# Performance work log

Hardware: AMD Instinct MI355X
Metric: run time of the kernel (lower is better)

Reference implementation:

```python
import jax, jax.numpy as jnp
import numpy as np

N_NODES = 10000
N_RAND_EDGES = 320000
IN_DIM = 256
HIDDEN = 64
HEADS = 8
OUT_DIM = 256
NEG_SLOPE = 0.2


def setup_inputs() -> dict:
    key = jax.random.key(0)
    ks = jax.random.split(key, 9)
    h = jax.random.normal(ks[0], (N_NODES, IN_DIM), dtype=jnp.float32)
    # random edges + self-loops so every dst has >=1 incoming edge
    src = jnp.concatenate([
        jax.random.randint(ks[1], (N_RAND_EDGES,), 0, N_NODES, dtype=jnp.int32),
        jnp.arange(N_NODES, dtype=jnp.int32)])
    dst = jnp.concatenate([
        jax.random.randint(ks[2], (N_RAND_EDGES,), 0, N_NODES, dtype=jnp.int32),
        jnp.arange(N_NODES, dtype=jnp.int32)])
    def glorot(k, shape):
        fan = shape[0] + shape[-1]
        s = jnp.sqrt(2.0 / fan).astype(jnp.float32)
        return jax.random.normal(k, shape, dtype=jnp.float32) * s
    W1 = glorot(ks[3], (IN_DIM, HEADS * HIDDEN))
    attn_l1 = glorot(ks[4], (HEADS, HIDDEN))
    attn_r1 = glorot(ks[5], (HEADS, HIDDEN))
    W2 = glorot(ks[6], (HEADS * HIDDEN, OUT_DIM))
    attn_l2 = glorot(ks[7], (1, OUT_DIM))
    attn_r2 = glorot(ks[8], (1, OUT_DIM))
    return {"h": h, "W1": W1, "attn_l1": attn_l1, "attn_r1": attn_r1,
            "W2": W2, "attn_l2": attn_l2, "attn_r2": attn_r2,
            "src": src, "dst": dst}


def gat_conv(x, W, attn_l, attn_r, src, dst, n_nodes):
    # x: [N, F_in]; W: [F_in, H*D]; attn_l/attn_r: [H, D]
    H, D = attn_l.shape
    feat = (x @ W).reshape(n_nodes, H, D)          # [N, H, D]
    el = jnp.einsum('nhd,hd->nh', feat, attn_l)    # [N, H]
    er = jnp.einsum('nhd,hd->nh', feat, attn_r)
    e = jax.nn.leaky_relu(el[src] + er[dst], NEG_SLOPE)  # [E, H]
    # edge softmax over incoming edges of each destination node
    m = jax.ops.segment_max(e, dst, num_segments=n_nodes)      # [N, H]
    ex = jnp.exp(e - m[dst])                                   # [E, H]
    denom = jax.ops.segment_sum(ex, dst, num_segments=n_nodes) # [N, H]
    alpha = ex / denom[dst]                                    # [E, H]
    out = jax.ops.segment_sum(alpha[:, :, None] * feat[src], dst,
                              num_segments=n_nodes)            # [N, H, D]
    return out.reshape(n_nodes, H * D)


def reference(h, W1, attn_l1, attn_r1, W2, attn_l2, attn_r2, src, dst):
    n = h.shape[0]
    x = gat_conv(h, W1, attn_l1, attn_r1, src, dst, n)   # [N, H*hidden]
    x = jax.nn.elu(x)
    out = gat_conv(x, W2, attn_l2, attn_r2, src, dst, n) # [N, out_dim]
    return out
```

## Files before the change

kernel.cpp:

```cpp
#include <hip/hip_runtime.h>
#include <hip/hip_bf16.h>

#define N_NODES 10000
#define IN_DIM 256
#define HID 512
#define HEADS 8
#define OUT_DIM 256
#define NEG 0.2f
#define CAP 128
#define WPREP_BLOCKS (((IN_DIM*HID)+(HID*OUT_DIM))/256)

typedef __hip_bfloat16 bf16;
typedef __attribute__((ext_vector_type(8))) short short8;
typedef __attribute__((ext_vector_type(4))) float f32x4;

__device__ __forceinline__ float ldm(const void* p, long i, int mode){
  if(mode) return ((const float*)p)[i];
  return __bfloat162float(((const bf16*)p)[i]);
}
__device__ __forceinline__ unsigned short f2bf(float f){
  bf16 b = __float2bfloat16(f);
  return *(unsigned short*)&b;
}
__device__ __forceinline__ float bflo(unsigned int u){ return __uint_as_float(u<<16); }
__device__ __forceinline__ float bfhi(unsigned int u){ return __uint_as_float(u&0xffff0000u); }

__global__ void detect_zero_k(const unsigned short* w1raw, int* mode, int* cnt,
                              float* el2, float* er2){
  int t = threadIdx.x;
  if(blockIdx.x==0){
    __shared__ int sbad;
    if(t==0) sbad=0;
    __syncthreads();
    int bad=0;
    for(int i=t;i<512;i+=256){
      unsigned int u = ((unsigned int)w1raw[i])<<16;
      float f = __uint_as_float(u);
      if(!(f==f) || fabsf(f) > 100.0f) bad++;
    }
    #pragma unroll
    for(int o=32;o>0;o>>=1) bad += __shfl_down(bad,o);
    if((t&63)==0) atomicAdd(&sbad, bad);
    __syncthreads();
    if(t==0) *mode = (sbad>10) ? 1 : 0;
  } else {
    int i = (blockIdx.x-1)*256 + t;
    if(i<N_NODES){ cnt[i]=0; el2[i]=0.f; er2[i]=0.f; }
  }
}

__global__ void prep2_k(const void* W1, const void* W2, unsigned short* wt1,
                        unsigned short* wt2, const int* modep,
                        const int* src, const int* dst, int* cnt, int* bucket, int E){
  int b = blockIdx.x, t = threadIdx.x;
  if(b < WPREP_BLOCKS){
    int md = *modep;
    long i = (long)b*256 + t;
    const long n1 = (long)IN_DIM*HID;
    if(i < n1){
      int k = (int)(i/HID), n = (int)(i%HID);
      unsigned short v = md ? f2bf(((const float*)W1)[i]) : ((const unsigned short*)W1)[i];
      wt1[(long)n*IN_DIM + k] = v;
    } else {
      long j = i - n1;
      int k = (int)(j/OUT_DIM), n = (int)(j%OUT_DIM);
      unsigned short v = md ? f2bf(((const float*)W2)[j]) : ((const unsigned short*)W2)[j];
      wt2[(long)n*HID + k] = v;
    }
  } else {
    int e = (b-WPREP_BLOCKS)*256 + t;
    if(e<E){
      int d = dst[e];
      int pos = atomicAdd(&cnt[d], 1);
      if(pos < CAP) bucket[(long)d*CAP + pos] = src[e];
    }
  }
}

__global__ __launch_bounds__(256) void gemm_k(const void* A, const unsigned short* Bt,
                                              unsigned short* C, int M, int N, int K,
                                              int asel, const int* modep,
                                              const void* al, const void* ar,
                                              float* el, float* er, int dmode){
  int md = *modep;
  int am = asel ? md : 0;
  __shared__ short As[64*40];
  __shared__ short Bs[64*40];
  __shared__ float led[64], ler[64];
  int t = threadIdx.x;
  int lane = t & 63, wave = t >> 6;
  int l15 = lane & 15, quad = lane >> 4;
  int wm = (wave>>1)*32, wn = (wave&1)*32;
  int mbase = blockIdx.y*64, nbase = blockIdx.x*64;

  f32x4 acc[2][2];
  #pragma unroll
  for(int i=0;i<2;i++)
    #pragma unroll
    for(int j=0;j<2;j++) acc[i][j] = (f32x4){0.f,0.f,0.f,0.f};

  int row = t>>2, kk = (t&3)*8;
  long arow = (long)(mbase+row)*K, brow = (long)(nbase+row)*K;
  bool av = (mbase+row) < M;
  const unsigned short* Ab = (const unsigned short*)A;
  const float* Af = (const float*)A;

  for(int k0=0;k0<K;k0+=32){
    short8 a = (short8){0,0,0,0,0,0,0,0};
    if(am){
      if(av){
        float4 x = *(const float4*)(Af + arow + k0 + kk);
        float4 y = *(const float4*)(Af + arow + k0 + kk + 4);
        a[0]=f2bf(x.x); a[1]=f2bf(x.y); a[2]=f2bf(x.z); a[3]=f2bf(x.w);
        a[4]=f2bf(y.x); a[5]=f2bf(y.y); a[6]=f2bf(y.z); a[7]=f2bf(y.w);
      }
    } else {
      if(av) a = *(const short8*)(Ab + arow + k0 + kk);
    }
    short8 b = *(const short8*)(Bt + brow + k0 + kk);
    __syncthreads();
    *(short8*)(As + row*40 + kk) = a;
    *(short8*)(Bs + row*40 + kk) = b;
    __syncthreads();
    short8 af[2], bfr[2];
    #pragma unroll
    for(int mi=0;mi<2;mi++) af[mi]  = *(short8*)(As + (wm + mi*16 + l15)*40 + quad*8);
    #pragma unroll
    for(int ni=0;ni<2;ni++) bfr[ni] = *(short8*)(Bs + (wn + ni*16 + l15)*40 + quad*8);
    #pragma unroll
    for(int mi=0;mi<2;mi++)
      #pragma unroll
      for(int ni=0;ni<2;ni++)
        acc[mi][ni] = __builtin_amdgcn_mfma_f32_16x16x32_bf16(af[mi], bfr[ni], acc[mi][ni], 0,0,0);
  }

  #pragma unroll
  for(int mi=0;mi<2;mi++){
    #pragma unroll
    for(int ni=0;ni<2;ni++){
      int grow0 = mbase + wm + mi*16 + quad*4;
      int gcol  = nbase + wn + ni*16 + l15;
      #pragma unroll
      for(int r=0;r<4;r++){
        int grow = grow0 + r;
        if(grow < M) C[(long)grow*N + gcol] = f2bf(acc[mi][ni][r]);
      }
    }
  }

  float avv[2], rvv[2];
  #pragma unroll
  for(int ni=0;ni<2;ni++){
    int gc = nbase + wn + ni*16 + l15;
    avv[ni] = ldm(al, gc, md);
    rvv[ni] = ldm(ar, gc, md);
  }
  __syncthreads();
  if(t<64){ led[t]=0.f; ler[t]=0.f; }
  __syncthreads();
  #pragma unroll
  for(int mi=0;mi<2;mi++){
    #pragma unroll
    for(int r=0;r<4;r++){
      float pl = acc[mi][0][r]*avv[0] + acc[mi][1][r]*avv[1];
      float pr = acc[mi][0][r]*rvv[0] + acc[mi][1][r]*rvv[1];
      #pragma unroll
      for(int o=1;o<16;o<<=1){ pl += __shfl_xor(pl,o); pr += __shfl_xor(pr,o); }
      if(l15==0){
        int lr = wm + mi*16 + quad*4 + r;
        atomicAdd(&led[lr], pl);
        atomicAdd(&ler[lr], pr);
      }
    }
  }
  __syncthreads();
  if(t<64){
    int grow = mbase + t;
    if(grow < M){
      if(dmode==1){
        el[(long)grow*HEADS + blockIdx.x] = led[t];
        er[(long)grow*HEADS + blockIdx.x] = ler[t];
      } else {
        atomicAdd(&el[grow], led[t]);
        atomicAdd(&er[grow], ler[t]);
      }
    }
  }
}

__global__ __launch_bounds__(64) void agg1_k(const unsigned short* fb, const float* el,
                       const float* er, const int* cnt, const int* bucket, unsigned short* x){
  int b = blockIdx.x;
  int ch = b / N_NODES;
  int n  = b - ch*N_NODES;
  int t = threadIdx.x;
  long off = (long)n*CAP;
  int deg = cnt[n]; if(deg>CAP) deg=CAP;
  __shared__ int sidx[CAP];
  __shared__ float wl[4][CAP];
  for(int i=t;i<deg;i+=64) sidx[i]=bucket[off+i];
  __syncthreads();
  int h0 = ch*4;
  float4 erv = *(const float4*)(er + (long)n*HEADS + h0);
  float pw0=0.f, pw1=0.f, pw2=0.f, pw3=0.f;
  for(int i=t;i<deg;i+=64){
    int s = sidx[i];
    float4 ev = *(const float4*)(el + (long)s*HEADS + h0);
    float e0 = ev.x + erv.x; e0 = e0>0.f?e0:NEG*e0;
    float e1 = ev.y + erv.y; e1 = e1>0.f?e1:NEG*e1;
    float e2 = ev.z + erv.z; e2 = e2>0.f?e2:NEG*e2;
    float e3 = ev.w + erv.w; e3 = e3>0.f?e3:NEG*e3;
    float wa = __expf(e0), wb = __expf(e1), wc = __expf(e2), wd = __expf(e3);
    wl[0][i]=wa; wl[1][i]=wb; wl[2][i]=wc; wl[3][i]=wd;
    pw0+=wa; pw1+=wb; pw2+=wc; pw3+=wd;
  }
  #pragma unroll
  for(int o=32;o>0;o>>=1){
    pw0 += __shfl_xor(pw0,o); pw1 += __shfl_xor(pw1,o);
    pw2 += __shfl_xor(pw2,o); pw3 += __shfl_xor(pw3,o);
  }
  float invs[4];
  invs[0] = pw0>0.f?1.f/pw0:0.f; invs[1] = pw1>0.f?1.f/pw1:0.f;
  invs[2] = pw2>0.f?1.f/pw2:0.f; invs[3] = pw3>0.f?1.f/pw3:0.f;
  __syncthreads();
  int hl = t>>4;
  int c0 = ch*256 + 4*t;
  const float* wsel = wl[hl];
  float inv = invs[hl];
  float a0=0.f,a1=0.f,a2=0.f,a3=0.f;
  #pragma unroll 4
  for(int i=0;i<deg;i++){
    int s = sidx[i];
    float w = wsel[i];
    uint2 u = *(const uint2*)(fb + (long)s*HID + c0);
    a0 += w*bflo(u.x); a1 += w*bfhi(u.x);
    a2 += w*bflo(u.y); a3 += w*bfhi(u.y);
  }
  a0*=inv; a1*=inv; a2*=inv; a3*=inv;
  a0 = a0>0.f ? a0 : __expf(a0)-1.f;
  a1 = a1>0.f ? a1 : __expf(a1)-1.f;
  a2 = a2>0.f ? a2 : __expf(a2)-1.f;
  a3 = a3>0.f ? a3 : __expf(a3)-1.f;
  uint2 o2;
  o2.x = (unsigned int)f2bf(a0) | ((unsigned int)f2bf(a1)<<16);
  o2.y = (unsigned int)f2bf(a2) | ((unsigned int)f2bf(a3)<<16);
  *(uint2*)(x + (long)n*HID + c0) = o2;
}

__global__ __launch_bounds__(64) void agg2_k(const unsigned short* fb, const float* el,
                       const float* er, const int* cnt, const int* bucket, void* out,
                       const int* modep){
  int md = *modep;
  int n = blockIdx.x, t = threadIdx.x;
  long off = (long)n*CAP;
  int deg = cnt[n]; if(deg>CAP) deg=CAP;
  __shared__ int sidx[CAP];
  __shared__ float wl[CAP];
  for(int i=t;i<deg;i+=64) sidx[i]=bucket[off+i];
  __syncthreads();
  float ern = er[n];
  float pw = 0.f;
  for(int i=t;i<deg;i+=64){
    int s = sidx[i];
    float e = el[s]+ern; e = e>0.f ? e : NEG*e;
    float w = __expf(e);
    wl[i]=w;
    pw += w;
  }
  #pragma unroll
  for(int o=32;o>0;o>>=1) pw += __shfl_xor(pw,o);
  float inv = pw>0.f ? 1.f/pw : 0.f;
  __syncthreads();
  int c0 = 4*t;
  float a0=0.f,a1=0.f,a2=0.f,a3=0.f;
  #pragma unroll 4
  for(int i=0;i<deg;i++){
    int s = sidx[i];
    float w = wl[i];
    uint2 u = *(const uint2*)(fb + (long)s*OUT_DIM + c0);
    a0 += w*bflo(u.x); a1 += w*bfhi(u.x);
    a2 += w*bflo(u.y); a3 += w*bfhi(u.y);
  }
  a0*=inv; a1*=inv; a2*=inv; a3*=inv;
  long oi = (long)n*OUT_DIM + c0;
  if(md){
    float4 fo; fo.x=a0; fo.y=a1; fo.z=a2; fo.w=a3;
    *(float4*)((float*)out + oi) = fo;
  } else {
    uint2 o2;
    o2.x = (unsigned int)f2bf(a0) | ((unsigned int)f2bf(a1)<<16);
    o2.y = (unsigned int)f2bf(a2) | ((unsigned int)f2bf(a3)<<16);
    *(uint2*)((unsigned short*)out + oi) = o2;
  }
}

extern "C" void kernel_launch(void* const* d_in, const int* in_sizes, int n_in,
                              void* d_out, int out_size, void* d_ws, size_t ws_size,
                              hipStream_t stream){
  (void)n_in; (void)out_size; (void)ws_size;
  const void* h_in = d_in[0];
  const void* W1   = d_in[1];
  const void* al1  = d_in[2];
  const void* ar1  = d_in[3];
  const void* W2   = d_in[4];
  const void* al2  = d_in[5];
  const void* ar2  = d_in[6];
  const int* src = (const int*)d_in[7];
  const int* dst = (const int*)d_in[8];
  int E = in_sizes[7];

  char* ws = (char*)d_ws;
  size_t o = 0;
  auto alloc = [&](size_t b){ size_t c=o; o += (b+255)&~(size_t)255; return c; };
  unsigned short* f1b  = (unsigned short*)(ws + alloc((size_t)N_NODES*HID*2));
  unsigned short* f2b  = (unsigned short*)(ws + alloc((size_t)N_NODES*OUT_DIM*2));
  unsigned short* xbuf = (unsigned short*)(ws + alloc((size_t)N_NODES*HID*2));
  unsigned short* wt1  = (unsigned short*)(ws + alloc((size_t)IN_DIM*HID*2));
  unsigned short* wt2  = (unsigned short*)(ws + alloc((size_t)HID*OUT_DIM*2));
  float* el1   = (float*)(ws + alloc((size_t)N_NODES*HEADS*4));
  float* er1   = (float*)(ws + alloc((size_t)N_NODES*HEADS*4));
  float* el2   = (float*)(ws + alloc((size_t)N_NODES*4));
  float* er2   = (float*)(ws + alloc((size_t)N_NODES*4));
  int* cnt     = (int*)(ws + alloc((size_t)N_NODES*4));
  int* bucket  = (int*)(ws + alloc((size_t)N_NODES*CAP*4));
  int* modep   = (int*)(ws + alloc(256));

  detect_zero_k<<<1+(N_NODES+255)/256,256,0,stream>>>(
      (const unsigned short*)W1, modep, cnt, el2, er2);
  prep2_k<<<WPREP_BLOCKS+(E+255)/256,256,0,stream>>>(
      W1, W2, wt1, wt2, modep, src, dst, cnt, bucket, E);

  gemm_k<<<dim3(HID/64,(N_NODES+63)/64),256,0,stream>>>(
      h_in, wt1, f1b, N_NODES, HID, IN_DIM, 1, modep, al1, ar1, el1, er1, 1);
  agg1_k<<<2*N_NODES,64,0,stream>>>(f1b, el1, er1, cnt, bucket, xbuf);

  gemm_k<<<dim3(OUT_DIM/64,(N_NODES+63)/64),256,0,stream>>>(
      xbuf, wt2, f2b, N_NODES, OUT_DIM, HID, 0, modep, al2, ar2, el2, er2, 2);
  agg2_k<<<N_NODES,64,0,stream>>>(f2b, el2, er2, cnt, bucket, d_out, modep);
}
```

Before: 184.1 us.

## Tile weight transpose through LDS and widen aggregation gathers to 16-byte loads

The weight-prep transpose now moves 64x64 tiles through shared memory with vectorized loads and stores, replacing the old uncoalesced scalar scatter. agg1 now runs one 128-thread block per node covering all 8 heads, where it used to run two 64-thread blocks per node. Each lane gathers 8 bf16 values with uint4 loads, the two waves split the edge list, and their partials are combined through LDS. agg2 also splits its edges across two half-waves with 16-byte loads and a shuffle reduction. This aims for fewer, wider gather transactions and less redundant edge-weight work, at the cost of fewer blocks and an extra reduction step.

```diff
diff --git a/kernel.cpp b/kernel.cpp
--- a/kernel.cpp
+++ b/kernel.cpp
@@ -8,7 +8,7 @@
 #define OUT_DIM 256
 #define NEG 0.2f
 #define CAP 128
-#define WPREP_BLOCKS (((IN_DIM*HID)+(HID*OUT_DIM))/256)
+#define WT_BLOCKS 64
 
 typedef __hip_bfloat16 bf16;
 typedef __attribute__((ext_vector_type(8))) short short8;
@@ -53,22 +53,43 @@
                         unsigned short* wt2, const int* modep,
                         const int* src, const int* dst, int* cnt, int* bucket, int E){
   int b = blockIdx.x, t = threadIdx.x;
-  if(b < WPREP_BLOCKS){
+  if(b < WT_BLOCKS){
     int md = *modep;
-    long i = (long)b*256 + t;
-    const long n1 = (long)IN_DIM*HID;
-    if(i < n1){
-      int k = (int)(i/HID), n = (int)(i%HID);
-      unsigned short v = md ? f2bf(((const float*)W1)[i]) : ((const unsigned short*)W1)[i];
-      wt1[(long)n*IN_DIM + k] = v;
+    __shared__ __align__(16) unsigned short tl[64*72];
+    int isW2 = (b>=32);
+    int bb = isW2 ? b-32 : b;
+    const void* W = isW2 ? W2 : W1;
+    unsigned short* wt = isW2 ? wt2 : wt1;
+    int K = isW2 ? HID : IN_DIM;
+    int N = isW2 ? OUT_DIM : HID;
+    int sh = isW2 ? 2 : 3;
+    int kt = bb >> sh, nt = bb & ((1<<sh)-1);
+    int r = t>>2, c0 = (t&3)<<4;
+    long srow = (long)(kt*64 + r)*N + nt*64 + c0;
+    unsigned short v[16] __attribute__((aligned(16)));
+    if(md){
+      const float* Wf = (const float*)W;
+      #pragma unroll
+      for(int j=0;j<16;j+=4){
+        float4 xv = *(const float4*)(Wf + srow + j);
+        v[j]=f2bf(xv.x); v[j+1]=f2bf(xv.y); v[j+2]=f2bf(xv.z); v[j+3]=f2bf(xv.w);
+      }
     } else {
-      long j = i - n1;
-      int k = (int)(j/OUT_DIM), n = (int)(j%OUT_DIM);
-      unsigned short v = md ? f2bf(((const float*)W2)[j]) : ((const unsigned short*)W2)[j];
-      wt2[(long)n*HID + k] = v;
-    }
+      const unsigned short* Wb = (const unsigned short*)W;
+      *(short8*)&v[0] = *(const short8*)(Wb+srow);
+      *(short8*)&v[8] = *(const short8*)(Wb+srow+8);
+    }
+    #pragma unroll
+    for(int j=0;j<16;j++) tl[(c0+j)*72 + r] = v[j];
+    __syncthreads();
+    int nn = t>>2, k0 = (t&3)<<4;
+    short8 o0 = *(short8*)&tl[nn*72+k0];
+    short8 o1 = *(short8*)&tl[nn*72+k0+8];
+    long drow = (long)(nt*64+nn)*K + kt*64 + k0;
+    *(short8*)(wt+drow)   = o0;
+    *(short8*)(wt+drow+8) = o1;
   } else {
-    int e = (b-WPREP_BLOCKS)*256 + t;
+    int e = (b-WT_BLOCKS)*256 + t;
     if(e<E){
       int d = dst[e];
       int pos = atomicAdd(&cnt[d], 1);
@@ -188,63 +209,92 @@
   }
 }
 
-__global__ __launch_bounds__(64) void agg1_k(const unsigned short* fb, const float* el,
+__global__ __launch_bounds__(128) void agg1_k(const unsigned short* fb, const float* el,
                        const float* er, const int* cnt, const int* bucket, unsigned short* x){
-  int b = blockIdx.x;
-  int ch = b / N_NODES;
-  int n  = b - ch*N_NODES;
+  int n = blockIdx.x;
   int t = threadIdx.x;
   long off = (long)n*CAP;
   int deg = cnt[n]; if(deg>CAP) deg=CAP;
   __shared__ int sidx[CAP];
-  __shared__ float wl[4][CAP];
-  for(int i=t;i<deg;i+=64) sidx[i]=bucket[off+i];
-  __syncthreads();
-  int h0 = ch*4;
-  float4 erv = *(const float4*)(er + (long)n*HEADS + h0);
-  float pw0=0.f, pw1=0.f, pw2=0.f, pw3=0.f;
-  for(int i=t;i<deg;i+=64){
+  __shared__ __align__(16) float swl[CAP*8];
+  __shared__ float pws[2][8];
+  __shared__ float sinv[8];
+  __shared__ __align__(16) float pacc[64][8];
+  for(int i=t;i<deg;i+=128) sidx[i]=bucket[off+i];
+  __syncthreads();
+  const float* erp = er + (long)n*HEADS;
+  float4 era = *(const float4*)erp, erb = *(const float4*)(erp+4);
+  float err8[8] = {era.x,era.y,era.z,era.w,erb.x,erb.y,erb.z,erb.w};
+  float pw[8];
+  #pragma unroll
+  for(int j=0;j<8;j++) pw[j]=0.f;
+  for(int i=t;i<deg;i+=128){
     int s = sidx[i];
-    float4 ev = *(const float4*)(el + (long)s*HEADS + h0);
-    float e0 = ev.x + erv.x; e0 = e0>0.f?e0:NEG*e0;
-    float e1 = ev.y + erv.y; e1 = e1>0.f?e1:NEG*e1;
-    float e2 = ev.z + erv.z; e2 = e2>0.f?e2:NEG*e2;
-    float e3 = ev.w + erv.w; e3 = e3>0.f?e3:NEG*e3;
-    float wa = __expf(e0), wb = __expf(e1), wc = __expf(e2), wd = __expf(e3);
-    wl[0][i]=wa; wl[1][i]=wb; wl[2][i]=wc; wl[3][i]=wd;
-    pw0+=wa; pw1+=wb; pw2+=wc; pw3+=wd;
-  }
-  #pragma unroll
-  for(int o=32;o>0;o>>=1){
-    pw0 += __shfl_xor(pw0,o); pw1 += __shfl_xor(pw1,o);
-    pw2 += __shfl_xor(pw2,o); pw3 += __shfl_xor(pw3,o);
-  }
-  float invs[4];
-  invs[0] = pw0>0.f?1.f/pw0:0.f; invs[1] = pw1>0.f?1.f/pw1:0.f;
-  invs[2] = pw2>0.f?1.f/pw2:0.f; invs[3] = pw3>0.f?1.f/pw3:0.f;
-  __syncthreads();
-  int hl = t>>4;
-  int c0 = ch*256 + 4*t;
-  const float* wsel = wl[hl];
-  float inv = invs[hl];
-  float a0=0.f,a1=0.f,a2=0.f,a3=0.f;
+    const float* ep = el + (long)s*HEADS;
+    float4 ea = *(const float4*)ep, eb = *(const float4*)(ep+4);
+    float ev[8] = {ea.x,ea.y,ea.z,ea.w,eb.x,eb.y,eb.z,eb.w};
+    float wv[8];
+    #pragma unroll
+    for(int j=0;j<8;j++){
+      float e = ev[j] + err8[j];
+      e = e>0.f ? e : NEG*e;
+      float w = __expf(e);
+      wv[j]=w; pw[j]+=w;
+    }
+    *(float4*)&swl[i*8]   = make_float4(wv[0],wv[1],wv[2],wv[3]);
+    *(float4*)&swl[i*8+4] = make_float4(wv[4],wv[5],wv[6],wv[7]);
+  }
+  #pragma unroll
+  for(int o=32;o>0;o>>=1)
+    #pragma unroll
+    for(int j=0;j<8;j++) pw[j]+=__shfl_xor(pw[j],o);
+  int wv_ = t>>6, l = t&63;
+  if(l==0){
+    #pragma unroll
+    for(int j=0;j<8;j++) pws[wv_][j]=pw[j];
+  }
+  __syncthreads();
+  if(t<8){ float s2 = pws[0][t]+pws[1][t]; sinv[t] = s2>0.f ? 1.f/s2 : 0.f; }
+  __syncthreads();
+  int h = l>>3;
+  int c0 = 8*l;
+  float a0=0.f,a1=0.f,a2=0.f,a3=0.f,a4=0.f,a5=0.f,a6=0.f,a7=0.f;
   #pragma unroll 4
-  for(int i=0;i<deg;i++){
+  for(int i=wv_; i<deg; i+=2){
     int s = sidx[i];
-    float w = wsel[i];
-    uint2 u = *(const uint2*)(fb + (long)s*HID + c0);
+    float w = swl[i*8+h];
+    uint4 u = *(const uint4*)(fb + (long)s*HID + c0);
     a0 += w*bflo(u.x); a1 += w*bfhi(u.x);
     a2 += w*bflo(u.y); a3 += w*bfhi(u.y);
-  }
-  a0*=inv; a1*=inv; a2*=inv; a3*=inv;
-  a0 = a0>0.f ? a0 : __expf(a0)-1.f;
-  a1 = a1>0.f ? a1 : __expf(a1)-1.f;
-  a2 = a2>0.f ? a2 : __expf(a2)-1.f;
-  a3 = a3>0.f ? a3 : __expf(a3)-1.f;
-  uint2 o2;
-  o2.x = (unsigned int)f2bf(a0) | ((unsigned int)f2bf(a1)<<16);
-  o2.y = (unsigned int)f2bf(a2) | ((unsigned int)f2bf(a3)<<16);
-  *(uint2*)(x + (long)n*HID + c0) = o2;
+    a4 += w*bflo(u.z); a5 += w*bfhi(u.z);
+    a6 += w*bflo(u.w); a7 += w*bfhi(u.w);
+  }
+  if(wv_==1){
+    *(float4*)&pacc[l][0] = make_float4(a0,a1,a2,a3);
+    *(float4*)&pacc[l][4] = make_float4(a4,a5,a6,a7);
+  }
+  __syncthreads();
+  if(wv_==0){
+    float4 q0 = *(float4*)&pacc[l][0], q1 = *(float4*)&pacc[l][4];
+    a0+=q0.x; a1+=q0.y; a2+=q0.z; a3+=q0.w;
+    a4+=q1.x; a5+=q1.y; a6+=q1.z; a7+=q1.w;
+    float inv = sinv[h];
+    a0*=inv; a1*=inv; a2*=inv; a3*=inv; a4*=inv; a5*=inv; a6*=inv; a7*=inv;
+    a0 = a0>0.f ? a0 : __expf(a0)-1.f;
+    a1 = a1>0.f ? a1 : __expf(a1)-1.f;
+    a2 = a2>0.f ? a2 : __expf(a2)-1.f;
+    a3 = a3>0.f ? a3 : __expf(a3)-1.f;
+    a4 = a4>0.f ? a4 : __expf(a4)-1.f;
+    a5 = a5>0.f ? a5 : __expf(a5)-1.f;
+    a6 = a6>0.f ? a6 : __expf(a6)-1.f;
+    a7 = a7>0.f ? a7 : __expf(a7)-1.f;
+    uint4 o4;
+    o4.x = (unsigned int)f2bf(a0) | ((unsigned int)f2bf(a1)<<16);
+    o4.y = (unsigned int)f2bf(a2) | ((unsigned int)f2bf(a3)<<16);
+    o4.z = (unsigned int)f2bf(a4) | ((unsigned int)f2bf(a5)<<16);
+    o4.w = (unsigned int)f2bf(a6) | ((unsigned int)f2bf(a7)<<16);
+    *(uint4*)(x + (long)n*HID + c0) = o4;
+  }
 }
 
 __global__ __launch_bounds__(64) void agg2_k(const unsigned short* fb, const float* el,
@@ -271,26 +321,39 @@
   for(int o=32;o>0;o>>=1) pw += __shfl_xor(pw,o);
   float inv = pw>0.f ? 1.f/pw : 0.f;
   __syncthreads();
-  int c0 = 4*t;
-  float a0=0.f,a1=0.f,a2=0.f,a3=0.f;
+  int half = t>>5, l = t&31;
+  int c0 = 8*l;
+  float a0=0.f,a1=0.f,a2=0.f,a3=0.f,a4=0.f,a5=0.f,a6=0.f,a7=0.f;
   #pragma unroll 4
-  for(int i=0;i<deg;i++){
+  for(int i=half; i<deg; i+=2){
     int s = sidx[i];
     float w = wl[i];
-    uint2 u = *(const uint2*)(fb + (long)s*OUT_DIM + c0);
+    uint4 u = *(const uint4*)(fb + (long)s*OUT_DIM + c0);
     a0 += w*bflo(u.x); a1 += w*bfhi(u.x);
     a2 += w*bflo(u.y); a3 += w*bfhi(u.y);
-  }
-  a0*=inv; a1*=inv; a2*=inv; a3*=inv;
-  long oi = (long)n*OUT_DIM + c0;
-  if(md){
-    float4 fo; fo.x=a0; fo.y=a1; fo.z=a2; fo.w=a3;
-    *(float4*)((float*)out + oi) = fo;
-  } else {
-    uint2 o2;
-    o2.x = (unsigned int)f2bf(a0) | ((unsigned int)f2bf(a1)<<16);
-    o2.y = (unsigned int)f2bf(a2) | ((unsigned int)f2bf(a3)<<16);
-    *(uint2*)((unsigned short*)out + oi) = o2;
+    a4 += w*bflo(u.z); a5 += w*bfhi(u.z);
+    a6 += w*bflo(u.w); a7 += w*bfhi(u.w);
+  }
+  a0 += __shfl_xor(a0,32); a1 += __shfl_xor(a1,32);
+  a2 += __shfl_xor(a2,32); a3 += __shfl_xor(a3,32);
+  a4 += __shfl_xor(a4,32); a5 += __shfl_xor(a5,32);
+  a6 += __shfl_xor(a6,32); a7 += __shfl_xor(a7,32);
+  if(half==0){
+    a0*=inv; a1*=inv; a2*=inv; a3*=inv; a4*=inv; a5*=inv; a6*=inv; a7*=inv;
+    long oi = (long)n*OUT_DIM + c0;
+    if(md){
+      float* of = (float*)out;
+      *(float4*)(of+oi)   = make_float4(a0,a1,a2,a3);
+      *(float4*)(of+oi+4) = make_float4(a4,a5,a6,a7);
+    } else {
+      unsigned short* ob = (unsigned short*)out;
+      uint4 o4;
+      o4.x = (unsigned int)f2bf(a0) | ((unsigned int)f2bf(a1)<<16);
+      o4.y = (unsigned int)f2bf(a2) | ((unsigned int)f2bf(a3)<<16);
+      o4.z = (unsigned int)f2bf(a4) | ((unsigned int)f2bf(a5)<<16);
+      o4.w = (unsigned int)f2bf(a6) | ((unsigned int)f2bf(a7)<<16);
+      *(uint4*)(ob+oi) = o4;
+    }
   }
 }
 
@@ -327,12 +390,12 @@
 
   detect_zero_k<<<1+(N_NODES+255)/256,256,0,stream>>>(
       (const unsigned short*)W1, modep, cnt, el2, er2);
-  prep2_k<<<WPREP_BLOCKS+(E+255)/256,256,0,stream>>>(
+  prep2_k<<<WT_BLOCKS+(E+255)/256,256,0,stream>>>(
       W1, W2, wt1, wt2, modep, src, dst, cnt, bucket, E);
 
   gemm_k<<<dim3(HID/64,(N_NODES+63)/64),256,0,stream>>>(
       h_in, wt1, f1b, N_NODES, HID, IN_DIM, 1, modep, al1, ar1, el1, er1, 1);
-  agg1_k<<<2*N_NODES,64,0,stream>>>(f1b, el1, er1, cnt, bucket, xbuf);
+  agg1_k<<<N_NODES,128,0,stream>>>(f1b, el1, er1, cnt, bucket, xbuf);
 
   gemm_k<<<dim3(OUT_DIM/64,(N_NODES+63)/64),256,0,stream>>>(
       xbuf, wt2, f2b, N_NODES, OUT_DIM, HID, 0, modep, al2, ar2, el2, er2, 2);
```

Result: no change. 186.4 us (+1.2%).
